# Performance work log

Hardware: AMD Instinct MI355X
Metric: run time of the kernel (lower is better)

## Reference

```python
import jax, jax.numpy as jnp
import numpy as np

B, N, D, H, F = 2, 2048, 1024, 16, 4096
HD = D // H


def setup_inputs() -> dict:
    key = jax.random.key(0)
    ks = jax.random.split(key, 16)
    s = 0.02
    x = jax.random.normal(ks[0], (B, N, D), jnp.float32)
    # tail padding: lengths in [N//2, N]; position >= length is padded
    lengths = jax.random.randint(ks[1], (B,), N // 2, N + 1)
    key_padding_mask = jnp.arange(N)[None, :] >= lengths[:, None]  # [B,N] bool, True = pad
    return {
        "x": x,
        "key_padding_mask": key_padding_mask,
        "ln1_g": jnp.ones((D,), jnp.float32),
        "ln1_b": jnp.zeros((D,), jnp.float32),
        "w_in": jax.random.normal(ks[2], (3 * D, D), jnp.float32) * s,  # packed QKV in_proj
        "b_in": jnp.zeros((3 * D,), jnp.float32),
        "w_out": jax.random.normal(ks[3], (D, D), jnp.float32) * s,
        "b_out": jnp.zeros((D,), jnp.float32),
        "ln2_g": jnp.ones((D,), jnp.float32),
        "ln2_b": jnp.zeros((D,), jnp.float32),
        "w1": jax.random.normal(ks[4], (F, D), jnp.float32) * s,
        "b1": jnp.zeros((F,), jnp.float32),
        "w2": jax.random.normal(ks[5], (D, F), jnp.float32) * s,
        "b2": jnp.zeros((D,), jnp.float32),
    }


def _layernorm(x, g, b):
    # source LayerNorm forces fp32 then casts back
    xf = x.astype(jnp.float32)
    m = xf.mean(-1, keepdims=True)
    v = xf.var(-1, keepdims=True)
    return (((xf - m) * jax.lax.rsqrt(v + 1e-5)) * g + b).astype(x.dtype)


def _quick_gelu(x):
    return x * jax.nn.sigmoid(1.702 * x)


def _block(x, key_padding_mask, ln1_g, ln1_b, w_in, b_in, w_out, b_out,
           ln2_g, ln2_b, w1, b1, w2, b2):
    n = x.shape[1]
    # combined mask: causal OR key-pad, with diagonal unmasked for padded query rows
    causal = jnp.triu(jnp.ones((n, n), bool), 1)                      # [N,N]
    combined = causal[None] | key_padding_mask[:, None, :]            # [B,N,N]
    diag = jnp.eye(n, dtype=bool)
    combined = combined & ~(diag[None] & key_padding_mask[:, :, None])

    # --- attention (pre-norm) ---
    xn = _layernorm(x, ln1_g, ln1_b)
    qkv = xn @ w_in.T + b_in                                          # [B,N,3D]
    q, k, v = jnp.split(qkv, 3, axis=-1)
    def heads(t):
        return t.reshape(x.shape[0], n, H, HD).transpose(0, 2, 1, 3)  # [B,H,N,hd]
    q, k, v = heads(q), heads(k), heads(v)
    scores = jnp.einsum('bhqd,bhkd->bhqk', q, k) / np.sqrt(HD)        # [B,H,N,N]
    scores = jnp.where(combined[:, None], -jnp.inf, scores)
    probs = jax.nn.softmax(scores, axis=-1)                           # [B,H,N,N]
    attn = jnp.einsum('bhqk,bhkd->bqhd', probs, v).reshape(x.shape[0], n, D)
    attn = attn @ w_out.T + b_out
    attn = jnp.where(key_padding_mask[:, :, None], 0.0, attn)         # zero padded queries
    weights = probs.mean(axis=1)                                      # need_weights avg over heads

    x = x + attn
    # --- FFN (pre-norm) ---
    xn = _layernorm(x, ln2_g, ln2_b)
    mlp = _quick_gelu(xn @ w1.T + b1) @ w2.T + b2
    x = x + mlp
    return x, weights


def reference(x, key_padding_mask, ln1_g, ln1_b, w_in, b_in, w_out, b_out,
              ln2_g, ln2_b, w1, b1, w2, b2):
    return _block(x, key_padding_mask, ln1_g, ln1_b, w_in, b_in, w_out, b_out,
                  ln2_g, ln2_b, w1, b1, w2, b2)
```

## Files before the change

### kernel.cpp

```cpp
#include <hip/hip_runtime.h>
#include <hip/hip_bf16.h>
#include <stdint.h>

#define DEVI __device__ __forceinline__

typedef __attribute__((ext_vector_type(8)))  short bf16x8;
typedef __attribute__((ext_vector_type(4)))  short s16x4;
typedef __attribute__((ext_vector_type(4)))  float f32x4;
typedef __attribute__((ext_vector_type(16))) float f32x16;
typedef __attribute__((ext_vector_type(2)))  unsigned int u32x2;
typedef __attribute__((ext_vector_type(4)))  unsigned int u32x4;

#define L2E 1.44269504088896f

DEVI unsigned short f2bf(float f){
  union{float f; unsigned int u;} v; v.f = f;
  unsigned int u = v.u;
  u = u + 0x7FFFu + ((u >> 16) & 1u);
  return (unsigned short)(u >> 16);
}

DEVI unsigned int cvt_pk_bf16(float lo, float hi){
  unsigned int r;
  asm("v_cvt_pk_bf16_f32 %0, %1, %2" : "=v"(r) : "v"(lo), "v"(hi));
  return r;
}

typedef const __attribute__((address_space(1))) unsigned int gq_t;
typedef __attribute__((address_space(3))) unsigned int lq_t;

DEVI void gl_lds16(const unsigned short* g, unsigned short* l){
  __builtin_amdgcn_global_load_lds((gq_t*)(uintptr_t)g, (lq_t*)(uintptr_t)l, 16, 0, 0);
}

__global__ void prep_len(const unsigned char* mask, int* lens){
  __shared__ int nz, cnt0, cnt1;
  int tid = threadIdx.x;
  if(tid == 0){ nz = 0; cnt0 = 0; cnt1 = 0; }
  __syncthreads();
  int loc = 0;
  for(int i = tid; i < 4096; i += 256) loc |= mask[i];
  if(loc) atomicOr(&nz, 1);
  __syncthreads();
  bool isu8 = (nz != 0);
  const int* m32 = (const int*)mask;
  int c0 = 0, c1 = 0;
  for(int i = tid; i < 2048; i += 256){
    int p0 = isu8 ? (int)mask[i]        : m32[i];
    int p1 = isu8 ? (int)mask[2048 + i] : m32[2048 + i];
    c0 += (p0 == 0);
    c1 += (p1 == 0);
  }
  atomicAdd(&cnt0, c0);
  atomicAdd(&cnt1, c1);
  __syncthreads();
  if(tid == 0){ lens[0] = cnt0; lens[1] = cnt1; }
}

__global__ void conv_bf16(const float* s, unsigned short* d, int n4){
  int i = blockIdx.x * 256 + threadIdx.x;
  if(i >= n4) return;
  f32x4 v = *(const f32x4*)(s + (size_t)i*4);
  s16x4 o;
  o[0]=(short)f2bf(v[0]); o[1]=(short)f2bf(v[1]);
  o[2]=(short)f2bf(v[2]); o[3]=(short)f2bf(v[3]);
  *(s16x4*)(d + (size_t)i*4) = o;
}

__global__ __launch_bounds__(256)
void ln_k(const float* x, const float* g, const float* b, unsigned short* y){
  int row = blockIdx.x, tid = threadIdx.x;
  const float* xr = x + (size_t)row*1024;
  f32x4 v = *(const f32x4*)(xr + tid*4);
  float s = v[0]+v[1]+v[2]+v[3];
#pragma unroll
  for(int o=1;o<64;o<<=1) s += __shfl_xor(s, o, 64);
  __shared__ float red[8];
  if((tid & 63) == 0) red[tid>>6] = s;
  __syncthreads();
  float mean = (red[0]+red[1]+red[2]+red[3]) * 0.0009765625f;
  float d0=v[0]-mean, d1=v[1]-mean, d2=v[2]-mean, d3=v[3]-mean;
  float s2 = d0*d0 + d1*d1 + d2*d2 + d3*d3;
#pragma unroll
  for(int o=1;o<64;o<<=1) s2 += __shfl_xor(s2, o, 64);
  if((tid & 63) == 0) red[4 + (tid>>6)] = s2;
  __syncthreads();
  float var = (red[4]+red[5]+red[6]+red[7]) * 0.0009765625f;
  float rstd = rsqrtf(var + 1e-5f);
  f32x4 gg = *(const f32x4*)(g + tid*4);
  f32x4 bb = *(const f32x4*)(b + tid*4);
  s16x4 o;
  o[0] = (short)f2bf(d0*rstd*gg[0] + bb[0]);
  o[1] = (short)f2bf(d1*rstd*gg[1] + bb[1]);
  o[2] = (short)f2bf(d2*rstd*gg[2] + bb[2]);
  o[3] = (short)f2bf(d3*rstd*gg[3] + bb[3]);
  *(s16x4*)(y + (size_t)row*1024 + tid*4) = o;
}

struct GemmP {
  const unsigned short* Wt;
  const unsigned short* Xa;
  int Nmat, K;
  const float* bias;
  const float* resid;
  const int* lens;
  float* outF;
  unsigned short* outB;
};

template<int EPI, int NB, int KB>
__global__ __launch_bounds__(256)
void gemm_k(GemmP p){
  constexpr int NF = NB/32;
  constexpr int CPR = KB/8;
  constexpr int NW = (NB*KB)/2048;
  constexpr int NX = (128*KB)/2048;
  __shared__ unsigned short lw[NB*KB];
  __shared__ unsigned short lx[128*KB];
  int nbn = p.Nmat / NB;
  int id = blockIdx.x;
  int cpx = gridDim.x >> 3;
  id = (id & 7)*cpx + (id >> 3);
  int bm = id / nbn, bn = id % nbn;
  int tid = threadIdx.x, lane = tid & 63, g = lane >> 4, l15 = lane & 15;
  int wave = tid >> 6, wm = wave & 1, wn = wave >> 1;

  const unsigned short* srcW[NW]; const unsigned short* srcX[NX];
  unsigned short* dstW[NW]; unsigned short* dstX[NX];
#pragma unroll
  for(int i=0;i<NW;++i){
    int slot = i*256 + tid, row = slot/CPR, c = slot%CPR, cs = c ^ (row & 7);
    srcW[i] = p.Wt + (size_t)(bn*NB + row)*p.K + cs*8;
    dstW[i] = lw + (i*256 + (tid & 192))*8;
  }
#pragma unroll
  for(int i=0;i<NX;++i){
    int slot = i*256 + tid, row = slot/CPR, c = slot%CPR, cs = c ^ (row & 7);
    srcX[i] = p.Xa + (size_t)(bm*128 + row)*p.K + cs*8;
    dstX[i] = lx + (i*256 + (tid & 192))*8;
  }

  f32x4 acc[NF][4];
#pragma unroll
  for(int a=0;a<NF;++a)
#pragma unroll
    for(int bb=0;bb<4;++bb)
#pragma unroll
      for(int e=0;e<4;++e) acc[a][bb][e] = 0.f;

  int iters = p.K / KB;
  for(int kt=0; kt<iters; ++kt){
#pragma unroll
    for(int i=0;i<NW;++i){
      gl_lds16(srcW[i], dstW[i]);
      srcW[i] += KB;
    }
#pragma unroll
    for(int i=0;i<NX;++i){
      gl_lds16(srcX[i], dstX[i]);
      srcX[i] += KB;
    }
    __syncthreads();
#pragma unroll
    for(int kc=0;kc<KB/32;++kc){
      bf16x8 af[NF], bfr[4];
#pragma unroll
      for(int nf=0;nf<NF;++nf){
        int row = wn*(16*NF) + nf*16 + l15;
        int ch = (kc*4 + g) ^ (row & 7);
        af[nf] = *(const bf16x8*)(lw + row*KB + ch*8);
      }
#pragma unroll
      for(int mf=0;mf<4;++mf){
        int row = wm*64 + mf*16 + l15;
        int ch = (kc*4 + g) ^ (row & 7);
        bfr[mf] = *(const bf16x8*)(lx + row*KB + ch*8);
      }
#pragma unroll
      for(int nf=0;nf<NF;++nf)
#pragma unroll
        for(int mf=0;mf<4;++mf)
          acc[nf][mf] = __builtin_amdgcn_mfma_f32_16x16x32_bf16(af[nf], bfr[mf], acc[nf][mf], 0, 0, 0);
    }
    __syncthreads();
  }

#pragma unroll
  for(int mf=0;mf<4;++mf){
    int m = bm*128 + wm*64 + mf*16 + l15;
#pragma unroll
    for(int nf=0;nf<NF;++nf){
      int n = bn*NB + wn*(16*NF) + nf*16 + g*4;
      f32x4 v = acc[nf][mf];
      f32x4 bz = *(const f32x4*)(p.bias + n);
      v = v + bz;
      if constexpr(EPI == 0){
        float sc = (n < 1024) ? 0.125f*L2E : 1.0f;
        s16x4 o;
#pragma unroll
        for(int e=0;e<4;++e) o[e] = (short)f2bf(v[e]*sc);
        *(s16x4*)(p.outB + (size_t)m*p.Nmat + n) = o;
      } else if constexpr(EPI == 1){
        int b_ = m >> 11, q = m & 2047;
        f32x4 r = *(const f32x4*)(p.resid + (size_t)m*1024 + n);
        if(q >= p.lens[b_]){ v[0]=0.f; v[1]=0.f; v[2]=0.f; v[3]=0.f; }
        v = v + r;
        *(f32x4*)(p.outF + (size_t)m*p.Nmat + n) = v;
      } else if constexpr(EPI == 2){
        s16x4 o;
#pragma unroll
        for(int e=0;e<4;++e){
          float sg = v[e]*__builtin_amdgcn_rcpf(1.f + exp2f(-1.702f*L2E*v[e]));
          o[e] = (short)f2bf(sg);
        }
        *(s16x4*)(p.outB + (size_t)m*p.Nmat + n) = o;
      } else {
        f32x4 r = *(const f32x4*)(p.resid + (size_t)m*p.Nmat + n);
        v = v + r;
        *(f32x4*)(p.outF + (size_t)m*p.Nmat + n) = v;
      }
    }
  }
}

__global__ __launch_bounds__(256)
void repack_vt(const unsigned short* qkv, unsigned short* vt){
  __shared__ unsigned short t[64*80];
  int id = blockIdx.x;
  int bh = id >> 5, nt = id & 31;
  int b = bh >> 4, h = bh & 15;
  int tid = threadIdx.x;
  int r = tid >> 2, c0 = (tid & 3)*16;
  const unsigned short* src = qkv + ((size_t)(b*2048 + nt*64 + r)*3072 + 2048 + h*64 + c0);
  bf16x8 v0 = *(const bf16x8*)(src);
  bf16x8 v1 = *(const bf16x8*)(src + 8);
  *(bf16x8*)(t + r*80 + c0) = v0;
  *(bf16x8*)(t + r*80 + c0 + 8) = v1;
  __syncthreads();
#pragma unroll
  for(int cc=0; cc<2; ++cc){
    int ci = cc*256 + tid;
    int hd = ci >> 3, nc = (ci & 7)*8;
    bf16x8 o;
#pragma unroll
    for(int i=0;i<8;++i) o[i] = (short)t[(nc+i)*80 + hd];
    *(bf16x8*)(vt + ((size_t)(bh*64 + hd)*2048 + nt*64 + nc)) = o;
  }
}

__global__ __launch_bounds__(256)
void attn_flash(const unsigned short* qkv, const unsigned short* vt,
                unsigned short* attnO, float* mrow, float* lrow, const int* lens)
{
  __shared__ unsigned short lk[2][64*64];
  __shared__ unsigned short lv[2][64*64];
  int id = blockIdx.x;
  int jj = id & 255;
  int bh = jj & 31;
  int qt = (id < 256) ? (15 - (jj >> 5)) : (jj >> 5);
  int b = bh >> 4, h = bh & 15;
  int tid = threadIdx.x, lane = tid & 63, wave = tid >> 6;
  int hi = lane >> 5, l31 = lane & 31;
  int q = qt*128 + wave*32 + l31;
  int len_b = lens[b];

  const unsigned short* qptr = qkv + ((size_t)(b*2048 + q)*3072 + h*64);
  bf16x8 qf[4];
#pragma unroll
  for(int ks=0;ks<4;++ks) qf[ks] = *(const bf16x8*)(qptr + ks*16 + hi*8);

  const unsigned short* srcK[2]; const unsigned short* srcV[2];
  int dof[2];
#pragma unroll
  for(int i=0;i<2;++i){
    int slot = i*256 + tid, row = slot >> 3, c = slot & 7, cs = c ^ (row & 7);
    srcK[i] = qkv + ((size_t)(b*2048 + row)*3072 + 1024 + h*64) + cs*8;
    srcV[i] = vt + ((size_t)(bh*64 + row)*2048) + cs*8;
    dof[i] = (i*256 + (tid & 192))*8;
  }

  f32x16 oacc[2];
#pragma unroll
  for(int a=0;a<2;++a)
#pragma unroll
    for(int e=0;e<16;++e) oacc[a][e] = 0.f;
  float mcur = -1e30f, lsum = 0.f;
  int ktmax = qt*2 + 1;

#pragma unroll
  for(int i=0;i<2;++i){
    gl_lds16(srcK[i], &lk[0][dof[i]]);
    gl_lds16(srcV[i], &lv[0][dof[i]]);
    srcK[i] += (size_t)64*3072;
    srcV[i] += 64;
  }
  __syncthreads();

  int buf = 0;
  for(int kt=0; kt<=ktmax; ++kt){
    if(kt < ktmax){
#pragma unroll
      for(int i=0;i<2;++i){
        gl_lds16(srcK[i], &lk[buf^1][dof[i]]);
        gl_lds16(srcV[i], &lv[buf^1][dof[i]]);
        srcK[i] += (size_t)64*3072;
        srcV[i] += 64;
      }
    }

    f32x16 s2[2];
#pragma unroll
    for(int kb=0;kb<2;++kb){
      f32x16 a;
#pragma unroll
      for(int e=0;e<16;++e) a[e] = 0.f;
      int row = kb*32 + l31;
#pragma unroll
      for(int ks=0;ks<4;++ks){
        int ch = (ks*2 + hi) ^ (row & 7);
        bf16x8 kf = *(const bf16x8*)(&lk[buf][0] + row*64 + ch*8);
        a = __builtin_amdgcn_mfma_f32_32x32x16_bf16(kf, qf[ks], a, 0, 0, 0);
      }
      s2[kb] = a;
    }

    float m0=-1e30f, m1=-1e30f, m2=-1e30f, m3=-1e30f;
    bool full = (kt*64 + 63 < qt*128 + wave*32) && (kt*64 + 64 <= len_b);
    if(full){
#pragma unroll
      for(int kb=0;kb<2;++kb)
#pragma unroll
        for(int r=0;r<16;r+=4){
          m0=fmaxf(m0,s2[kb][r+0]); m1=fmaxf(m1,s2[kb][r+1]);
          m2=fmaxf(m2,s2[kb][r+2]); m3=fmaxf(m3,s2[kb][r+3]);
        }
    } else {
#pragma unroll
      for(int kb=0;kb<2;++kb)
#pragma unroll
        for(int r=0;r<16;++r){
          int key = kt*64 + kb*32 + (r&3) + 8*(r>>2) + 4*hi;
          bool ok = (key == q) || ((key < q) && (key < len_b));
          float tv = ok ? s2[kb][r] : -1e30f;
          s2[kb][r] = tv;
          if((r&3)==0) m0=fmaxf(m0,tv); else if((r&3)==1) m1=fmaxf(m1,tv);
          else if((r&3)==2) m2=fmaxf(m2,tv); else m3=fmaxf(m3,tv);
        }
    }
    float tmax = fmaxf(fmaxf(m0,m1), fmaxf(m2,m3));
    tmax = fmaxf(tmax, __shfl_xor(tmax, 32, 64));

    if(!__all(tmax <= mcur + 8.f)){
      float mnew = fmaxf(mcur, tmax);
      float fsc = exp2f(mcur - mnew);
      lsum *= fsc;
#pragma unroll
      for(int a=0;a<2;++a)
#pragma unroll
        for(int e=0;e<16;++e) oacc[a][e] *= fsc;
      mcur = mnew;
    }
    float r0=0.f, r1=0.f, r2=0.f, r3=0.f;
#pragma unroll
    for(int kb=0;kb<2;++kb)
#pragma unroll
      for(int r=0;r<16;++r){
        float pv = exp2f(s2[kb][r] - mcur);
        s2[kb][r] = pv;
        if((r&3)==0) r0+=pv; else if((r&3)==1) r1+=pv;
        else if((r&3)==2) r2+=pv; else r3+=pv;
      }
    float rsum = (r0+r1)+(r2+r3);
    rsum += __shfl_xor(rsum, 32, 64);
    lsum += rsum;

#pragma unroll
    for(int ks=0;ks<4;++ks){
      int kb = ks >> 1, r0i = (ks & 1)*8;
      unsigned int a0 = cvt_pk_bf16(s2[kb][r0i+0], s2[kb][r0i+1]);
      unsigned int a1 = cvt_pk_bf16(s2[kb][r0i+2], s2[kb][r0i+3]);
      unsigned int a2 = cvt_pk_bf16(s2[kb][r0i+4], s2[kb][r0i+5]);
      unsigned int a3 = cvt_pk_bf16(s2[kb][r0i+6], s2[kb][r0i+7]);
      unsigned int b0 = __shfl_xor(a0, 32, 64);
      unsigned int b1 = __shfl_xor(a1, 32, 64);
      unsigned int b2 = __shfl_xor(a2, 32, 64);
      unsigned int b3 = __shfl_xor(a3, 32, 64);
      union { u32x4 u; bf16x8 s8; } pw;
      pw.u[0] = hi ? b2 : a0;
      pw.u[1] = hi ? b3 : a1;
      pw.u[2] = hi ? a2 : b0;
      pw.u[3] = hi ? a3 : b1;
#pragma unroll
      for(int af=0;af<2;++af){
        int vrow = af*32 + l31;
        int ch = (ks*2 + hi) ^ (vrow & 7);
        bf16x8 vf = *(const bf16x8*)(&lv[buf][0] + vrow*64 + ch*8);
        oacc[af] = __builtin_amdgcn_mfma_f32_32x32x16_bf16(vf, pw.s8, oacc[af], 0, 0, 0);
      }
    }
    __syncthreads();
    buf ^= 1;
  }

  float rl = __builtin_amdgcn_rcpf(lsum);
  if(hi == 0){
    mrow[(size_t)bh*2048 + q] = mcur;
    lrow[(size_t)bh*2048 + q] = lsum;
  }
  unsigned short* obase = attnO + ((size_t)(b*2048 + q)*1024 + h*64);
#pragma unroll
  for(int af=0;af<2;++af)
#pragma unroll
    for(int grp=0; grp<4; ++grp){
      int hd0 = af*32 + grp*8 + hi*4;
      u32x2 st;
      st[0] = cvt_pk_bf16(oacc[af][grp*4+0]*rl, oacc[af][grp*4+1]*rl);
      st[1] = cvt_pk_bf16(oacc[af][grp*4+2]*rl, oacc[af][grp*4+3]*rl);
      *(u32x2*)(obase + hd0) = st;
    }
}

__global__ void prep_c(const float* mrow, const float* lrow, float* cbuf){
  int i = blockIdx.x*256 + threadIdx.x;
  cbuf[i] = exp2f(-mrow[i]) * __builtin_amdgcn_rcpf(lrow[i]);
}

__global__ __launch_bounds__(256)
void attn_weights(const unsigned short* qkv, const float* cbuf,
                  float* wout, const int* lens)
{
  int id = blockIdx.x;
  int kt = id & 15, qt = (id >> 4) & 15, b = id >> 8;
  int tid = threadIdx.x;
  float* wtile = wout + ((size_t)(b*2048 + qt*128))*2048 + kt*128;

  if(kt > qt){
    f32x4 z; z[0]=0.f; z[1]=0.f; z[2]=0.f; z[3]=0.f;
#pragma unroll
    for(int i=0;i<8;++i){
      float* p = wtile + (size_t)(i*16 + (tid>>4))*2048 + (tid&15)*8;
      *(f32x4*)p = z; *(f32x4*)(p+4) = z;
    }
    return;
  }

  __shared__ unsigned short lk[2][128*64];
  __shared__ unsigned short lq[2][128*64];
  int lane = tid & 63, wave = tid >> 6, hi = lane >> 5, l31 = lane & 31;
  int len_b = lens[b];
  int q_abs = qt*128 + wave*32 + l31;

  const float* cb = cbuf + (size_t)(b*16)*2048 + q_abs;
  float ccs[16];
#pragma unroll
  for(int h=0;h<16;++h) ccs[h] = cb[(size_t)h*2048];

  const unsigned short* srcK[4]; const unsigned short* srcQ[4]; int dA[4];
#pragma unroll
  for(int i=0;i<4;++i){
    int d = i*256 + tid, row = d >> 3, c = d & 7, cs = c ^ (row & 7);
    srcK[i] = qkv + ((size_t)(b*2048 + kt*128 + row)*3072 + 1024) + cs*8;
    srcQ[i] = qkv + ((size_t)(b*2048 + qt*128 + row)*3072) + cs*8;
    dA[i] = d*8;
  }

  float wacc[4][16];
#pragma unroll
  for(int ksub=0;ksub<4;++ksub)
#pragma unroll
    for(int r=0;r<16;++r) wacc[ksub][r] = 0.f;

#pragma unroll
  for(int i=0;i<4;++i){
    gl_lds16(srcK[i], &lk[0][dA[i]]);
    gl_lds16(srcQ[i], &lq[0][dA[i]]);
  }
  __syncthreads();

  int buf = 0;
  for(int h=0;h<16;++h){
    if(h < 15){
#pragma unroll
      for(int i=0;i<4;++i){
        gl_lds16(srcK[i] + (h+1)*64, &lk[buf^1][dA[i]]);
        gl_lds16(srcQ[i] + (h+1)*64, &lq[buf^1][dA[i]]);
      }
    }
    bf16x8 qf[4];
#pragma unroll
    for(int ks=0;ks<4;++ks){
      int row = wave*32 + l31;
      int ch = (ks*2 + hi) ^ (row & 7);
      qf[ks] = *(const bf16x8*)(&lq[buf][0] + row*64 + ch*8);
    }
    float cc = ccs[h];
#pragma unroll
    for(int ksub=0;ksub<4;++ksub){
      f32x16 sc;
#pragma unroll
      for(int e=0;e<16;++e) sc[e] = 0.f;
#pragma unroll
      for(int ks=0;ks<4;++ks){
        int row = ksub*32 + l31;
        int ch = (ks*2 + hi) ^ (row & 7);
        bf16x8 kf = *(const bf16x8*)(&lk[buf][0] + row*64 + ch*8);
        sc = __builtin_amdgcn_mfma_f32_32x32x16_bf16(kf, qf[ks], sc, 0, 0, 0);
      }
#pragma unroll
      for(int r=0;r<16;++r)
        wacc[ksub][r] += exp2f(sc[r]) * cc;
    }
    __syncthreads();
    buf ^= 1;
  }

#pragma unroll
  for(int ksub=0;ksub<4;++ksub)
#pragma unroll
    for(int rg=0;rg<4;++rg){
      f32x4 v;
#pragma unroll
      for(int e=0;e<4;++e){
        int key_abs = kt*128 + ksub*32 + rg*8 + hi*4 + e;
        bool ok = (key_abs == q_abs) || ((key_abs < q_abs) && (key_abs < len_b));
        v[e] = ok ? wacc[ksub][rg*4 + e]*0.0625f : 0.f;
      }
      *(f32x4*)(wtile + (size_t)(wave*32 + l31)*2048 + ksub*32 + rg*8 + hi*4) = v;
    }
}

extern "C" void kernel_launch(void* const* d_in, const int* in_sizes, int n_in,
                              void* d_out, int out_size, void* d_ws, size_t ws_size,
                              hipStream_t stream)
{
  const float* x     = (const float*)d_in[0];
  const unsigned char* mask = (const unsigned char*)d_in[1];
  const float* ln1g  = (const float*)d_in[2];
  const float* ln1b  = (const float*)d_in[3];
  const float* w_in  = (const float*)d_in[4];
  const float* b_in  = (const float*)d_in[5];
  const float* w_out = (const float*)d_in[6];
  const float* b_out = (const float*)d_in[7];
  const float* ln2g  = (const float*)d_in[8];
  const float* ln2b  = (const float*)d_in[9];
  const float* w1    = (const float*)d_in[10];
  const float* b1    = (const float*)d_in[11];
  const float* w2    = (const float*)d_in[12];
  const float* b2    = (const float*)d_in[13];
  float* out = (float*)d_out;

  char* ws = (char*)d_ws;
  size_t off = 0;
  auto take = [&](size_t bytes)->char*{
    char* p = ws + off; off += (bytes + 255) & ~(size_t)255; return p;
  };
  int* lens            = (int*)take(256);
  unsigned short* wq   = (unsigned short*)take((size_t)3072*1024*2);
  unsigned short* wo   = (unsigned short*)take((size_t)1024*1024*2);
  unsigned short* w1c  = (unsigned short*)take((size_t)4096*1024*2);
  unsigned short* w2c  = (unsigned short*)take((size_t)1024*4096*2);
  unsigned short* xn   = (unsigned short*)take((size_t)4096*1024*2);
  unsigned short* qkv  = (unsigned short*)take((size_t)4096*3072*2);
  unsigned short* vt   = (unsigned short*)take((size_t)32*64*2048*2);
  float* mrow          = (float*)take((size_t)32*2048*4);
  float* lrow          = (float*)take((size_t)32*2048*4);
  float* cbuf          = (float*)take((size_t)32*2048*4);
  unsigned short* aO   = (unsigned short*)take((size_t)4096*1024*2);
  float* x1            = (float*)take((size_t)4096*1024*4);
  unsigned short* hmid = (unsigned short*)take((size_t)4096*4096*2);

  prep_len<<<1,256,0,stream>>>(mask, lens);
  conv_bf16<<<3072,256,0,stream>>>(w_in, wq, 786432);
  conv_bf16<<<1024,256,0,stream>>>(w_out, wo, 262144);
  conv_bf16<<<4096,256,0,stream>>>(w1, w1c, 1048576);
  conv_bf16<<<4096,256,0,stream>>>(w2, w2c, 1048576);
  ln_k<<<4096,256,0,stream>>>(x, ln1g, ln1b, xn);

  GemmP p1{wq, xn, 3072, 1024, b_in, nullptr, nullptr, nullptr, qkv};
  gemm_k<0,128,64><<<768,256,0,stream>>>(p1);
  repack_vt<<<1024,256,0,stream>>>(qkv, vt);
  attn_flash<<<512,256,0,stream>>>(qkv, vt, aO, mrow, lrow, lens);
  prep_c<<<256,256,0,stream>>>(mrow, lrow, cbuf);
  attn_weights<<<512,256,0,stream>>>(qkv, cbuf, out + 4194304, lens);

  GemmP p2{wo, aO, 1024, 1024, b_out, x, lens, x1, nullptr};
  gemm_k<1,64,128><<<512,256,0,stream>>>(p2);
  ln_k<<<4096,256,0,stream>>>(x1, ln2g, ln2b, xn);
  GemmP p3{w1c, xn, 4096, 1024, b1, nullptr, nullptr, nullptr, hmid};
  gemm_k<2,128,64><<<1024,256,0,stream>>>(p3);
  GemmP p4{w2c, hmid, 1024, 4096, b2, x1, nullptr, out, nullptr};
  gemm_k<3,64,128><<<512,256,0,stream>>>(p4);
}
```

Measured before the change: 320.0 us.

## Give each wave its own head and skip causal tiles per 32-row query slice

The attention kernel now assigns each wave an independent (batch, head) pair over a 32-row query slice, with a private LDS K/V tile per wave, instead of four waves sharing a 128-row query tile. Each wave loops only over the key tiles its own causal range needs, which removes block-level barriers and some wasted masked tiles. The cost is the loss of double buffering: loads are issued and then waited on before compute each tile, so memory latency is exposed and K/V is no longer shared across waves. s_setprio is added around the MFMA sections.

```diff
diff --git a/kernel.cpp b/kernel.cpp
--- a/kernel.cpp
+++ b/kernel.cpp
@@ -252,32 +252,28 @@
 void attn_flash(const unsigned short* qkv, const unsigned short* vt,
                 unsigned short* attnO, float* mrow, float* lrow, const int* lens)
 {
-  __shared__ unsigned short lk[2][64*64];
-  __shared__ unsigned short lv[2][64*64];
+  __shared__ unsigned short lk[4][64*64];
+  __shared__ unsigned short lv[4][64*64];
   int id = blockIdx.x;
-  int jj = id & 255;
-  int bh = jj & 31;
-  int qt = (id < 256) ? (15 - (jj >> 5)) : (jj >> 5);
+  int wave = threadIdx.x >> 6, lane = threadIdx.x & 63;
+  int hi = lane >> 5, l31 = lane & 31;
+  int j = (id < 256) ? (63 - (id >> 3)) : ((id - 256) >> 3);
+  int bh = (id & 7)*4 + wave;
   int b = bh >> 4, h = bh & 15;
-  int tid = threadIdx.x, lane = tid & 63, wave = tid >> 6;
-  int hi = lane >> 5, l31 = lane & 31;
-  int q = qt*128 + wave*32 + l31;
+  int q = j*32 + l31;
   int len_b = lens[b];
+  int ntiles = (j + 2) >> 1;
 
   const unsigned short* qptr = qkv + ((size_t)(b*2048 + q)*3072 + h*64);
   bf16x8 qf[4];
 #pragma unroll
   for(int ks=0;ks<4;++ks) qf[ks] = *(const bf16x8*)(qptr + ks*16 + hi*8);
 
-  const unsigned short* srcK[2]; const unsigned short* srcV[2];
-  int dof[2];
-#pragma unroll
-  for(int i=0;i<2;++i){
-    int slot = i*256 + tid, row = slot >> 3, c = slot & 7, cs = c ^ (row & 7);
-    srcK[i] = qkv + ((size_t)(b*2048 + row)*3072 + 1024 + h*64) + cs*8;
-    srcV[i] = vt + ((size_t)(bh*64 + row)*2048) + cs*8;
-    dof[i] = (i*256 + (tid & 192))*8;
-  }
+  int cs = (lane & 7) ^ (lane >> 3);
+  const unsigned short* kSrc = qkv + ((size_t)(b*2048 + (lane>>3))*3072 + 1024 + h*64) + cs*8;
+  const unsigned short* vSrc = vt + ((size_t)(bh*64 + (lane>>3))*2048) + cs*8;
+  unsigned short* kDst = &lk[wave][0];
+  unsigned short* vDst = &lv[wave][0];
 
   f32x16 oacc[2];
 #pragma unroll
@@ -285,30 +281,19 @@
 #pragma unroll
     for(int e=0;e<16;++e) oacc[a][e] = 0.f;
   float mcur = -1e30f, lsum = 0.f;
-  int ktmax = qt*2 + 1;
-
-#pragma unroll
-  for(int i=0;i<2;++i){
-    gl_lds16(srcK[i], &lk[0][dof[i]]);
-    gl_lds16(srcV[i], &lv[0][dof[i]]);
-    srcK[i] += (size_t)64*3072;
-    srcV[i] += 64;
-  }
-  __syncthreads();
-
-  int buf = 0;
-  for(int kt=0; kt<=ktmax; ++kt){
-    if(kt < ktmax){
-#pragma unroll
-      for(int i=0;i<2;++i){
-        gl_lds16(srcK[i], &lk[buf^1][dof[i]]);
-        gl_lds16(srcV[i], &lv[buf^1][dof[i]]);
-        srcK[i] += (size_t)64*3072;
-        srcV[i] += 64;
-      }
-    }
+
+  for(int t=0; t<ntiles; ++t){
+#pragma unroll
+    for(int i=0;i<8;++i){
+      gl_lds16(kSrc + (size_t)i*8*3072, kDst + i*512);
+      gl_lds16(vSrc + (size_t)i*8*2048, vDst + i*512);
+    }
+    kSrc += (size_t)64*3072;
+    vSrc += 64;
+    asm volatile("s_waitcnt vmcnt(0)" ::: "memory");
 
     f32x16 s2[2];
+    __builtin_amdgcn_s_setprio(1);
 #pragma unroll
     for(int kb=0;kb<2;++kb){
       f32x16 a;
@@ -318,14 +303,15 @@
 #pragma unroll
       for(int ks=0;ks<4;++ks){
         int ch = (ks*2 + hi) ^ (row & 7);
-        bf16x8 kf = *(const bf16x8*)(&lk[buf][0] + row*64 + ch*8);
+        bf16x8 kf = *(const bf16x8*)(kDst + row*64 + ch*8);
         a = __builtin_amdgcn_mfma_f32_32x32x16_bf16(kf, qf[ks], a, 0, 0, 0);
       }
       s2[kb] = a;
     }
+    __builtin_amdgcn_s_setprio(0);
 
     float m0=-1e30f, m1=-1e30f, m2=-1e30f, m3=-1e30f;
-    bool full = (kt*64 + 63 < qt*128 + wave*32) && (kt*64 + 64 <= len_b);
+    bool full = (t*64 + 63 < j*32) && (t*64 + 64 <= len_b);
     if(full){
 #pragma unroll
       for(int kb=0;kb<2;++kb)
@@ -339,7 +325,7 @@
       for(int kb=0;kb<2;++kb)
 #pragma unroll
         for(int r=0;r<16;++r){
-          int key = kt*64 + kb*32 + (r&3) + 8*(r>>2) + 4*hi;
+          int key = t*64 + kb*32 + (r&3) + 8*(r>>2) + 4*hi;
           bool ok = (key == q) || ((key < q) && (key < len_b));
           float tv = ok ? s2[kb][r] : -1e30f;
           s2[kb][r] = tv;
@@ -374,6 +360,7 @@
     rsum += __shfl_xor(rsum, 32, 64);
     lsum += rsum;
 
+    __builtin_amdgcn_s_setprio(1);
 #pragma unroll
     for(int ks=0;ks<4;++ks){
       int kb = ks >> 1, r0i = (ks & 1)*8;
@@ -394,12 +381,12 @@
       for(int af=0;af<2;++af){
         int vrow = af*32 + l31;
         int ch = (ks*2 + hi) ^ (vrow & 7);
-        bf16x8 vf = *(const bf16x8*)(&lv[buf][0] + vrow*64 + ch*8);
+        bf16x8 vf = *(const bf16x8*)(vDst + vrow*64 + ch*8);
         oacc[af] = __builtin_amdgcn_mfma_f32_32x32x16_bf16(vf, pw.s8, oacc[af], 0, 0, 0);
       }
     }
-    __syncthreads();
-    buf ^= 1;
+    __builtin_amdgcn_s_setprio(0);
+    asm volatile("s_waitcnt lgkmcnt(0)" ::: "memory");
   }
 
   float rl = __builtin_amdgcn_rcpf(lsum);
```

Result: slower. 332.6 us (+3.9%).
